# Kernel optimization log

Hardware: AMD Instinct MI355X
Metric: run time of the kernel (lower is better)

The kernel has to match this reference:

```python
import jax, jax.numpy as jnp
import numpy as np

B, C, H, W = 8, 256, 64, 64
EPS = 1e-5


def _mk_conv_bn(key, oc, ic):
    k = jax.random.split(key, 6)
    return dict(
        w=jax.random.normal(k[0], (oc, ic), jnp.float32) * 0.01,  # trunc-normal approx, stddev 0.01
        b=jnp.zeros((oc,), jnp.float32),
        s=jax.random.uniform(k[1], (oc,), jnp.float32, 0.5, 1.5),   # BN scale
        t=jax.random.normal(k[2], (oc,), jnp.float32) * 0.1,        # BN shift
        m=jax.random.normal(k[3], (oc,), jnp.float32) * 0.1,        # BN running mean
        v=jax.random.uniform(k[4], (oc,), jnp.float32, 0.5, 1.5),   # BN running var
    )


def setup_inputs() -> dict:
    key = jax.random.key(0)
    ks = jax.random.split(key, 6)
    d = {"x": jax.random.normal(ks[0], (B, C, H, W), jnp.float32)}
    for i, (oc, ic) in zip([1, 2, 3, 4], [(C // 8, C), (C // 8, C), (C // 2, C), (C, C // 2)]):
        p = _mk_conv_bn(ks[i], oc, ic)
        for name, val in p.items():
            d[f"{name}{i}"] = val
    d["gamma"] = jnp.asarray(0.5, jnp.float32)
    return d


def _cbn(x, w, b, s, t, m, v, relu=True):
    # conv1x1 + BatchNorm(eval) [+ ReLU]; dropout is identity at inference
    y = jnp.einsum('bchw,oc->bohw', x, w) + b[None, :, None, None]
    scale = (s / jnp.sqrt(v + EPS))[None, :, None, None]
    y = (y - m[None, :, None, None]) * scale + t[None, :, None, None]
    return jax.nn.relu(y) if relu else y


def _maxpool2(x):
    b, c, h, w = x.shape
    return x.reshape(b, c, h // 2, 2, w // 2, 2).max(axis=(3, 5))


def reference(x, w1, b1, s1, t1, m1, v1, w2, b2, s2, t2, m2, v2,
              w3, b3, s3, t3, m3, v3, w4, b4, s4, t4, m4, v4, gamma):
    b, c, h, w = x.shape
    f = _maxpool2(_cbn(x, w1, b1, s1, t1, m1, v1))   # (B, C/8, H/2, W/2)
    g = _cbn(x, w2, b2, s2, t2, m2, v2)              # (B, C/8, H, W)
    hh = _maxpool2(_cbn(x, w3, b3, s3, t3, m3, v3))  # (B, C/2, H/2, W/2)
    hw, hw4 = h * w, (h // 2) * (w // 2)
    f = f.reshape(b, c // 8, hw4).transpose(0, 2, 1)  # (B, HW/4, C/8)
    g = g.reshape(b, c // 8, hw)                      # (B, C/8, HW)
    s = jnp.einsum('bnk,bkm->bnm', f, g)              # (B, HW/4, HW)
    beta = jax.nn.softmax(s, axis=1)                  # softmax over dim=1, as in source
    hh = hh.reshape(b, c // 2, hw4)                   # (B, C/2, HW/4)
    o = jnp.einsum('bcn,bnm->bcm', hh, beta).reshape(b, c // 2, h, w)
    out = _cbn(o, w4, b4, s4, t4, m4, v4, relu=False)
    return gamma * out + x
```

## Files before the change

kernel.cpp:

```cpp
#include <hip/hip_runtime.h>
#include <hip/hip_bf16.h>

#define HW   4096
#define HW4  1024
#define EPS  1e-5f
#define SM_SHIFT 20.0f

typedef __attribute__((ext_vector_type(8)))  short    bf16x8;
typedef __attribute__((ext_vector_type(4)))  float    f32x4;

__device__ __forceinline__ short f2bs(float f) {
    union { float f; unsigned u; } v; v.f = f;
    unsigned r = v.u + 0x7FFFu + ((v.u >> 16) & 1u);
    return (short)(r >> 16);
}
__device__ __forceinline__ unsigned pk2(float a, float b) {
    unsigned r;
    asm("v_cvt_pk_bf16_f32 %0, %1, %2" : "=v"(r) : "v"(a), "v"(b));
    return r;
}
__device__ __forceinline__ int swz64(int r, int c)  { return (r << 6) + ((c ^ (r & 7))  << 3); }
__device__ __forceinline__ int swz128(int r, int c) { return (r << 7) + ((c ^ (r & 15)) << 3); }
__device__ __forceinline__ int p40(int r, int c)    { return r * 40 + c * 8; }

__device__ __forceinline__ void bar_lgk() {
    asm volatile("s_waitcnt lgkmcnt(0)" ::: "memory");
    __builtin_amdgcn_s_barrier();
    __builtin_amdgcn_sched_barrier(0);
}

__global__ __launch_bounds__(512) void conv123pool(
    const float* __restrict__ x,
    const float* __restrict__ w1, const float* __restrict__ b1, const float* __restrict__ s1,
    const float* __restrict__ t1, const float* __restrict__ m1, const float* __restrict__ v1,
    const float* __restrict__ w2, const float* __restrict__ b2, const float* __restrict__ s2,
    const float* __restrict__ t2, const float* __restrict__ m2, const float* __restrict__ v2,
    const float* __restrict__ w3, const float* __restrict__ b3, const float* __restrict__ s3,
    const float* __restrict__ t3, const float* __restrict__ m3, const float* __restrict__ v3,
    const float* __restrict__ w4,
    short* __restrict__ w4T,
    short* __restrict__ gbufT, short* __restrict__ fbufT, short* __restrict__ hhbuf)
{
    __shared__ __align__(16) short Wl[4 * 192 * 64];
    __shared__ __align__(16) short Xl[2 * 128 * 64];
    __shared__ float alB[192], beB[192];

    const int t = threadIdx.x;
    const int lane = t & 63, wv = t >> 6;
    const int quad = lane >> 4, l16 = lane & 15;
    const int ptile = blockIdx.x;
    const int bz    = blockIdx.y;
    const int pBase = ptile * 128;
    const int wcol  = (wv & 1) * 32;
    const int woch  = (wv >> 1) * 48;

    const int xp2 = (t & 63) * 2, xkg = t >> 6;
    const float* xBase = x + ((size_t)bz * 256 + xkg * 8) * HW + pBase + xp2;

    float2 fvA[8], fvB[8];
    #pragma unroll
    for (int j = 0; j < 8; ++j) fvA[j] = *(const float2*)(xBase + (size_t)j * HW);

    if (bz == 0) {
        int idx = (ptile * 512 + t) * 2;
        float2 a = *(const float2*)(w4 + idx);
        short2 o; o.x = f2bs(a.x); o.y = f2bs(a.y);
        *(short2*)&w4T[idx] = o;
    }

    if (t < 192) {
        int j = t;
        float pb, ps, ptv, pm, pv;
        if (j < 32)      { pb = b1[j]; ps = s1[j]; ptv = t1[j]; pm = m1[j]; pv = v1[j]; }
        else if (j < 64) { int c = j - 32; pb = b2[c]; ps = s2[c]; ptv = t2[c]; pm = m2[c]; pv = v2[c]; }
        else             { int c = j - 64; pb = b3[c]; ps = s3[c]; ptv = t3[c]; pm = m3[c]; pv = v3[c]; }
        float al = ps * rsqrtf(pv + EPS);
        alB[t] = al; beB[t] = (pb - pm) * al + ptv;
    }

    #pragma unroll
    for (int kc = 0; kc < 4; ++kc) {
        #pragma unroll
        for (int i = 0; i < 2; ++i) {
            int idx = t + i * 512;
            if (i == 0 || t < 256) {
                int oc = idx >> 2, kb = (idx & 3) * 16;
                const float* wp = (oc < 32) ? (w1 + oc * 256)
                                : (oc < 64) ? (w2 + (oc - 32) * 256)
                                            : (w3 + (oc - 64) * 256);
                wp += kc * 64 + kb;
                float4 a = *(const float4*)(wp);
                float4 b = *(const float4*)(wp + 4);
                float4 c = *(const float4*)(wp + 8);
                float4 d = *(const float4*)(wp + 12);
                bf16x8 lo, hi;
                lo[0]=f2bs(a.x); lo[1]=f2bs(a.y); lo[2]=f2bs(a.z); lo[3]=f2bs(a.w);
                lo[4]=f2bs(b.x); lo[5]=f2bs(b.y); lo[6]=f2bs(b.z); lo[7]=f2bs(b.w);
                hi[0]=f2bs(c.x); hi[1]=f2bs(c.y); hi[2]=f2bs(c.z); hi[3]=f2bs(c.w);
                hi[4]=f2bs(d.x); hi[5]=f2bs(d.y); hi[6]=f2bs(d.z); hi[7]=f2bs(d.w);
                *(bf16x8*)&Wl[kc * 12288 + swz64(oc, (kb >> 3))]     = lo;
                *(bf16x8*)&Wl[kc * 12288 + swz64(oc, (kb >> 3) + 1)] = hi;
            }
        }
    }

    const f32x4 fzero = {0.f, 0.f, 0.f, 0.f};
    f32x4 acc[3][4];
    #pragma unroll
    for (int i = 0; i < 3; ++i)
        #pragma unroll
        for (int j = 0; j < 4; ++j) acc[i][j] = fzero;

    const int ptOff0 = wcol, ptOff1 = wcol + 16, ptOff2 = wcol + 64, ptOff3 = wcol + 80;

#define K1_COMMIT(XB, CUR)                                                            \
    {   bf16x8 va, vb;                                                                \
        _Pragma("unroll")                                                             \
        for (int j2 = 0; j2 < 8; ++j2) { va[j2] = f2bs(CUR[j2].x); vb[j2] = f2bs(CUR[j2].y); } \
        *(bf16x8*)&Xl[(XB) * 8192 + swz64(xp2,     xkg)] = va;                        \
        *(bf16x8*)&Xl[(XB) * 8192 + swz64(xp2 + 1, xkg)] = vb;                        \
    }
#define K1_PREF(KC, NXT)                                                              \
    {   const float* xn = xBase + (size_t)((KC) * 64) * HW;                           \
        _Pragma("unroll")                                                             \
        for (int j2 = 0; j2 < 8; ++j2) NXT[j2] = *(const float2*)(xn + (size_t)j2 * HW); \
    }
#define K1_MFMA(XB, KC)                                                               \
    _Pragma("unroll")                                                                 \
    for (int kk = 0; kk < 2; ++kk) {                                                  \
        bf16x8 bfr[4];                                                                \
        bfr[0] = *(const bf16x8*)&Xl[(XB) * 8192 + swz64(ptOff0 + l16, kk * 4 + quad)]; \
        bfr[1] = *(const bf16x8*)&Xl[(XB) * 8192 + swz64(ptOff1 + l16, kk * 4 + quad)]; \
        bfr[2] = *(const bf16x8*)&Xl[(XB) * 8192 + swz64(ptOff2 + l16, kk * 4 + quad)]; \
        bfr[3] = *(const bf16x8*)&Xl[(XB) * 8192 + swz64(ptOff3 + l16, kk * 4 + quad)]; \
        _Pragma("unroll")                                                             \
        for (int tt = 0; tt < 3; ++tt) {                                              \
            bf16x8 afr = *(const bf16x8*)&Wl[(KC) * 12288 + swz64(woch + tt*16 + l16, kk*4 + quad)]; \
            _Pragma("unroll")                                                         \
            for (int pt = 0; pt < 4; ++pt)                                            \
                acc[tt][pt] = __builtin_amdgcn_mfma_f32_16x16x32_bf16(afr, bfr[pt], acc[tt][pt], 0, 0, 0); \
        }                                                                             \
    }

    K1_COMMIT(0, fvA)  K1_PREF(1, fvB)  bar_lgk();  K1_MFMA(0, 0)
    K1_COMMIT(1, fvB)  K1_PREF(2, fvA)  bar_lgk();  K1_MFMA(1, 1)
    K1_COMMIT(0, fvA)  K1_PREF(3, fvB)  bar_lgk();  K1_MFMA(0, 2)
    K1_COMMIT(1, fvB)                   bar_lgk();  K1_MFMA(1, 3)

#undef K1_COMMIT
#undef K1_PREF
#undef K1_MFMA

    #pragma unroll
    for (int tt = 0; tt < 3; ++tt) {
        #pragma unroll
        for (int r = 0; r < 4; ++r) {
            int j = woch + tt * 16 + quad * 4 + r;
            float al = alB[j], be = beB[j];
            float y[4];
            y[0] = fmaxf(acc[tt][0][r] * al + be, 0.f);
            y[1] = fmaxf(acc[tt][1][r] * al + be, 0.f);
            y[2] = fmaxf(acc[tt][2][r] * al + be, 0.f);
            y[3] = fmaxf(acc[tt][3][r] * al + be, 0.f);
            if (j >= 32 && j < 64) {
                size_t mb = (size_t)bz * 4096 + pBase;
                int kk = j - 32;
                gbufT[(mb + ptOff0 + l16) * 32 + kk] = f2bs(y[0]);
                gbufT[(mb + ptOff1 + l16) * 32 + kk] = f2bs(y[1]);
                gbufT[(mb + ptOff2 + l16) * 32 + kk] = f2bs(y[2]);
                gbufT[(mb + ptOff3 + l16) * 32 + kk] = f2bs(y[3]);
            } else {
                #pragma unroll
                for (int c = 0; c < 2; ++c) {
                    float v  = fmaxf(y[c], y[c + 2]);
                    float po = fmaxf(v, __shfl_xor(v, 1));
                    if ((l16 & 1) == 0) {
                        int col = wcol + c * 16 + l16;
                        int n = ptile * 32 + (col >> 1);
                        if (j < 32) fbufT[((size_t)bz * 1024 + n) * 32 + j] = f2bs(po);
                        else        hhbuf[((size_t)bz * 128 + (j - 64)) * HW4 + n] = f2bs(po);
                    }
                }
            }
        }
    }
}

__global__ __launch_bounds__(256, 2) void attn_conv4(
    const short* __restrict__ gbufT,
    const short* __restrict__ fbufT,
    const short* __restrict__ hhbuf,
    const float* __restrict__ x,
    const short* __restrict__ w4T, const float* __restrict__ b4, const float* __restrict__ s4,
    const float* __restrict__ t4, const float* __restrict__ m4, const float* __restrict__ v4,
    const float* __restrict__ gamma, float* __restrict__ out)
{
    __shared__ __align__(16) short smem[24576];
    __shared__ float alB4[256], beB4[256];
    __shared__ float Zl[128];
    short* o_l  = smem;
    short* Wl4  = smem + 8192;
    float* mrg  = (float*)(smem + 8192);
    short* sTp  = smem + (threadIdx.x >> 6) * 2560;

    const int t = threadIdx.x;
    const int lane = t & 63, wv = t >> 6;
    const int quad = lane >> 4, l16 = lane & 15;
    const int ci = wv >> 1, ni = wv & 1;
    const int nstrip = ni * 32, cbase = ci * 64;
    const int bz = blockIdx.y;
    const int m0 = blockIdx.x * 64;
    const f32x4 fzero = {0.f, 0.f, 0.f, 0.f};

    {
        float al = s4[t] * rsqrtf(v4[t] + EPS);
        alB4[t] = al; beB4[t] = (b4[t] - m4[t]) * al + t4[t];
    }

    const short* fT = fbufT + (size_t)bz * 1024 * 32;
    const short* hB = hhbuf + (size_t)bz * 128 * HW4;

    bf16x8 bg[4];
    #pragma unroll
    for (int mt = 0; mt < 4; ++mt)
        bg[mt] = *(const bf16x8*)&gbufT[((size_t)bz * 4096 + m0 + mt * 16 + l16) * 32 + quad * 8];

    bf16x8 frA[2], frB[2], hhA[4], hhB[4];
    frA[0] = *(const bf16x8*)&fT[(size_t)(nstrip + l16) * 32 + quad * 8];
    frA[1] = *(const bf16x8*)&fT[(size_t)(nstrip + 16 + l16) * 32 + quad * 8];
    #pragma unroll
    for (int ct = 0; ct < 4; ++ct)
        hhA[ct] = *(const bf16x8*)(hB + (size_t)(cbase + ct * 16 + l16) * HW4 + nstrip + quad * 8);

    float psum[4] = {0.f, 0.f, 0.f, 0.f};
    f32x4 oacc[4][4];
    #pragma unroll
    for (int a = 0; a < 4; ++a)
        #pragma unroll
        for (int b = 0; b < 4; ++b) oacc[a][b] = fzero;

    const int mr0 = l16 * 40, mr1 = (16 + l16) * 40, mr2 = (32 + l16) * 40, mr3 = (48 + l16) * 40;
    const int mrow[4] = {mr0, mr1, mr2, mr3};

    int n0n = 64;

#define ABODY(CURF, NXTF, CURH, NXTH)                                                 \
    {                                                                                 \
        f32x4 sacc0[4], sacc1[4];                                                     \
        _Pragma("unroll")                                                             \
        for (int mt = 0; mt < 4; ++mt)                                                \
            sacc0[mt] = __builtin_amdgcn_mfma_f32_16x16x32_bf16(CURF[0], bg[mt], fzero, 0, 0, 0); \
        _Pragma("unroll")                                                             \
        for (int mt = 0; mt < 4; ++mt)                                                \
            sacc1[mt] = __builtin_amdgcn_mfma_f32_16x16x32_bf16(CURF[1], bg[mt], fzero, 0, 0, 0); \
        NXTF[0] = *(const bf16x8*)&fT[(size_t)(n0n + nstrip + l16) * 32 + quad * 8];  \
        NXTF[1] = *(const bf16x8*)&fT[(size_t)(n0n + nstrip + 16 + l16) * 32 + quad * 8]; \
        _Pragma("unroll")                                                             \
        for (int mt = 0; mt < 4; ++mt) {                                              \
            float e0 = __expf(sacc0[mt][0] - SM_SHIFT);                               \
            float e1 = __expf(sacc0[mt][1] - SM_SHIFT);                               \
            float e2 = __expf(sacc0[mt][2] - SM_SHIFT);                               \
            float e3 = __expf(sacc0[mt][3] - SM_SHIFT);                               \
            float g0 = __expf(sacc1[mt][0] - SM_SHIFT);                               \
            float g1 = __expf(sacc1[mt][1] - SM_SHIFT);                               \
            float g2 = __expf(sacc1[mt][2] - SM_SHIFT);                               \
            float g3 = __expf(sacc1[mt][3] - SM_SHIFT);                               \
            psum[mt] += ((e0 + e1) + (e2 + e3)) + ((g0 + g1) + (g2 + g3));            \
            uint2 ev0; ev0.x = pk2(e0, e1); ev0.y = pk2(e2, e3);                      \
            uint2 ev1; ev1.x = pk2(g0, g1); ev1.y = pk2(g2, g3);                      \
            *(uint2*)&sTp[mrow[mt] + quad * 4]      = ev0;                            \
            *(uint2*)&sTp[mrow[mt] + 16 + quad * 4] = ev1;                            \
        }                                                                             \
        _Pragma("unroll")                                                             \
        for (int mt = 0; mt < 4; ++mt) {                                              \
            bf16x8 bfrag = *(const bf16x8*)&sTp[mrow[mt] + quad * 8];                 \
            _Pragma("unroll")                                                         \
            for (int ct = 0; ct < 4; ++ct)                                            \
                oacc[ct][mt] = __builtin_amdgcn_mfma_f32_16x16x32_bf16(CURH[ct], bfrag, oacc[ct][mt], 0, 0, 0); \
        }                                                                             \
        _Pragma("unroll")                                                             \
        for (int ct = 0; ct < 4; ++ct)                                                \
            NXTH[ct] = *(const bf16x8*)(hB + (size_t)(cbase + ct * 16 + l16) * HW4 + n0n + nstrip + quad * 8); \
        n0n = (n0n + 64) & 1023;                                                      \
    }

    for (int it2 = 0; it2 < 8; ++it2) {
        ABODY(frA, frB, hhA, hhB)
        ABODY(frB, frA, hhB, hhA)
    }
#undef ABODY

    #pragma unroll
    for (int mt = 0; mt < 4; ++mt) {
        psum[mt] += __shfl_xor(psum[mt], 16);
        psum[mt] += __shfl_xor(psum[mt], 32);
    }

    bar_lgk();

    if (ci == 0 && quad == 0) {
        #pragma unroll
        for (int mt = 0; mt < 4; ++mt) Zl[ni * 64 + mt * 16 + l16] = psum[mt];
    }
    if (ni == 1) {
        #pragma unroll
        for (int ct = 0; ct < 4; ++ct)
            #pragma unroll
            for (int mt = 0; mt < 4; ++mt)
                #pragma unroll
                for (int r = 0; r < 4; ++r)
                    mrg[(cbase + ct * 16 + quad * 4 + r) * 64 + mt * 16 + l16] = oacc[ct][mt][r];
    }
    bar_lgk();

    if (ni == 0) {
        #pragma unroll
        for (int mt = 0; mt < 4; ++mt) {
            float iv = 1.0f / (Zl[mt * 16 + l16] + Zl[64 + mt * 16 + l16]);
            #pragma unroll
            for (int ct = 0; ct < 4; ++ct) {
                short4 ov;
                #pragma unroll
                for (int r = 0; r < 4; ++r) {
                    float v = oacc[ct][mt][r]
                            + mrg[(cbase + ct * 16 + quad * 4 + r) * 64 + mt * 16 + l16];
                    ((short*)&ov)[r] = f2bs(v * iv);
                }
                *(short4*)&o_l[swz128(mt * 16 + l16, ci * 8 + ct * 2 + (quad >> 1)) + (quad & 1) * 4] = ov;
            }
        }
    }

    f32x4 acc4[4][4];
    #pragma unroll
    for (int i = 0; i < 4; ++i)
        #pragma unroll
        for (int j = 0; j < 4; ++j) acc4[i][j] = fzero;

    const int wrow = t >> 2, wcid = t & 3;
    bf16x8 Wr[4];
    #pragma unroll
    for (int g = 0; g < 4; ++g)
        Wr[g] = *(const bf16x8*)(w4T + (g * 64 + wrow) * 128 + wcid * 8);

    #pragma unroll
    for (int k0i = 0; k0i < 4; ++k0i) {
        const int k0 = k0i * 32;
        bar_lgk();
        #pragma unroll
        for (int g = 0; g < 4; ++g)
            *(bf16x8*)&Wl4[p40(g * 64 + wrow, wcid)] = Wr[g];
        if (k0i < 3) {
            #pragma unroll
            for (int g = 0; g < 4; ++g)
                Wr[g] = *(const bf16x8*)(w4T + (g * 64 + wrow) * 128 + k0 + 32 + wcid * 8);
        }
        bar_lgk();
        bf16x8 bfr[4];
        #pragma unroll
        for (int mt = 0; mt < 4; ++mt)
            bfr[mt] = *(const bf16x8*)&o_l[swz128(mt * 16 + l16, (k0 >> 3) + quad)];
        #pragma unroll
        for (int ot = 0; ot < 4; ++ot) {
            bf16x8 afr = *(const bf16x8*)&Wl4[p40(wv * 64 + ot * 16 + l16, quad)];
            #pragma unroll
            for (int mt = 0; mt < 4; ++mt)
                acc4[ot][mt] = __builtin_amdgcn_mfma_f32_16x16x32_bf16(afr, bfr[mt], acc4[ot][mt], 0, 0, 0);
        }
    }

    float gm = gamma[0];
    #pragma unroll
    for (int ot = 0; ot < 4; ++ot) {
        #pragma unroll
        for (int r = 0; r < 4; ++r) {
            int oc = wv * 64 + ot * 16 + quad * 4 + r;
            float al = alB4[oc], be = beB4[oc];
            #pragma unroll
            for (int mt = 0; mt < 4; ++mt) {
                int p = m0 + mt * 16 + l16;
                float y  = acc4[ot][mt][r] * al + be;
                float xo = x[((size_t)bz * 256 + oc) * HW + p];
                out[((size_t)bz * 256 + oc) * HW + p] = gm * y + xo;
            }
        }
    }
}

extern "C" void kernel_launch(void* const* d_in, const int* in_sizes, int n_in,
                              void* d_out, int out_size, void* d_ws, size_t ws_size,
                              hipStream_t stream)
{
    const float* x  = (const float*)d_in[0];
    const float* w1 = (const float*)d_in[1];
    const float* b1 = (const float*)d_in[2];
    const float* s1 = (const float*)d_in[3];
    const float* t1 = (const float*)d_in[4];
    const float* m1 = (const float*)d_in[5];
    const float* v1 = (const float*)d_in[6];
    const float* w2 = (const float*)d_in[7];
    const float* b2 = (const float*)d_in[8];
    const float* s2 = (const float*)d_in[9];
    const float* t2 = (const float*)d_in[10];
    const float* m2 = (const float*)d_in[11];
    const float* v2 = (const float*)d_in[12];
    const float* w3 = (const float*)d_in[13];
    const float* b3 = (const float*)d_in[14];
    const float* s3 = (const float*)d_in[15];
    const float* t3 = (const float*)d_in[16];
    const float* m3 = (const float*)d_in[17];
    const float* v3 = (const float*)d_in[18];
    const float* w4 = (const float*)d_in[19];
    const float* b4 = (const float*)d_in[20];
    const float* s4 = (const float*)d_in[21];
    const float* t4 = (const float*)d_in[22];
    const float* m4 = (const float*)d_in[23];
    const float* v4 = (const float*)d_in[24];
    const float* gm = (const float*)d_in[25];
    float* out = (float*)d_out;

    short* gbufT = (short*)d_ws;
    short* fbufT = gbufT + (size_t)8 * 4096 * 32;
    short* hhbuf = fbufT + (size_t)8 * 1024 * 32;
    short* w4T   = hhbuf + (size_t)8 * 128 * 1024;

    conv123pool<<<dim3(32, 8), 512, 0, stream>>>(
        x, w1, b1, s1, t1, m1, v1, w2, b2, s2, t2, m2, v2, w3, b3, s3, t3, m3, v3,
        w4, w4T, gbufT, fbufT, hhbuf);
    attn_conv4<<<dim3(64, 8), 256, 0, stream>>>(
        gbufT, fbufT, hhbuf, x, w4T, b4, s4, t4, m4, v4, gm, out);
}
```

Baseline: 164.8 us.

## Compute softmax denominators via MFMA with ones, use packed bf16 converts

Replaces the per-lane scalar exp-sum accumulation and cross-lane shuffle reduction with an extra MFMA per tile that multiplies a ones fragment by the bf16 probability fragment. The column sums then come out of the matrix core and stay consistent with the rounded bf16 values used in the PV product. Software bf16 rounding in the projection kernel is swapped for the packed v_cvt_pk_bf16_f32 instruction. The attention kernel's occupancy hint is dropped and the custom barriers become __syncthreads. The extra MFMA adds matrix-core work, and relaxing launch bounds may change register allocation and occupancy.

```diff
diff --git a/kernel.cpp b/kernel.cpp
--- a/kernel.cpp
+++ b/kernel.cpp
@@ -8,6 +8,7 @@
 
 typedef __attribute__((ext_vector_type(8)))  short    bf16x8;
 typedef __attribute__((ext_vector_type(4)))  float    f32x4;
+typedef __attribute__((ext_vector_type(4)))  unsigned u32x4;
 
 __device__ __forceinline__ short f2bs(float f) {
     union { float f; unsigned u; } v; v.f = f;
@@ -64,8 +65,8 @@
     if (bz == 0) {
         int idx = (ptile * 512 + t) * 2;
         float2 a = *(const float2*)(w4 + idx);
-        short2 o; o.x = f2bs(a.x); o.y = f2bs(a.y);
-        *(short2*)&w4T[idx] = o;
+        unsigned o = pk2(a.x, a.y);
+        *(unsigned*)&w4T[idx] = o;
     }
 
     if (t < 192) {
@@ -93,13 +94,10 @@
                 float4 b = *(const float4*)(wp + 4);
                 float4 c = *(const float4*)(wp + 8);
                 float4 d = *(const float4*)(wp + 12);
-                bf16x8 lo, hi;
-                lo[0]=f2bs(a.x); lo[1]=f2bs(a.y); lo[2]=f2bs(a.z); lo[3]=f2bs(a.w);
-                lo[4]=f2bs(b.x); lo[5]=f2bs(b.y); lo[6]=f2bs(b.z); lo[7]=f2bs(b.w);
-                hi[0]=f2bs(c.x); hi[1]=f2bs(c.y); hi[2]=f2bs(c.z); hi[3]=f2bs(c.w);
-                hi[4]=f2bs(d.x); hi[5]=f2bs(d.y); hi[6]=f2bs(d.z); hi[7]=f2bs(d.w);
-                *(bf16x8*)&Wl[kc * 12288 + swz64(oc, (kb >> 3))]     = lo;
-                *(bf16x8*)&Wl[kc * 12288 + swz64(oc, (kb >> 3) + 1)] = hi;
+                *(u32x4*)&Wl[kc * 12288 + swz64(oc, (kb >> 3))] =
+                    (u32x4){pk2(a.x,a.y), pk2(a.z,a.w), pk2(b.x,b.y), pk2(b.z,b.w)};
+                *(u32x4*)&Wl[kc * 12288 + swz64(oc, (kb >> 3) + 1)] =
+                    (u32x4){pk2(c.x,c.y), pk2(c.z,c.w), pk2(d.x,d.y), pk2(d.z,d.w)};
             }
         }
     }
@@ -114,11 +112,14 @@
     const int ptOff0 = wcol, ptOff1 = wcol + 16, ptOff2 = wcol + 64, ptOff3 = wcol + 80;
 
 #define K1_COMMIT(XB, CUR)                                                            \
-    {   bf16x8 va, vb;                                                                \
-        _Pragma("unroll")                                                             \
-        for (int j2 = 0; j2 < 8; ++j2) { va[j2] = f2bs(CUR[j2].x); vb[j2] = f2bs(CUR[j2].y); } \
-        *(bf16x8*)&Xl[(XB) * 8192 + swz64(xp2,     xkg)] = va;                        \
-        *(bf16x8*)&Xl[(XB) * 8192 + swz64(xp2 + 1, xkg)] = vb;                        \
+    {   u32x4 va, vb;                                                                 \
+        _Pragma("unroll")                                                             \
+        for (int w2i = 0; w2i < 4; ++w2i) {                                           \
+            va[w2i] = pk2(CUR[2*w2i].x, CUR[2*w2i+1].x);                              \
+            vb[w2i] = pk2(CUR[2*w2i].y, CUR[2*w2i+1].y);                              \
+        }                                                                             \
+        *(u32x4*)&Xl[(XB) * 8192 + swz64(xp2,     xkg)] = va;                         \
+        *(u32x4*)&Xl[(XB) * 8192 + swz64(xp2 + 1, xkg)] = vb;                         \
     }
 #define K1_PREF(KC, NXT)                                                              \
     {   const float* xn = xBase + (size_t)((KC) * 64) * HW;                           \
@@ -186,7 +187,7 @@
     }
 }
 
-__global__ __launch_bounds__(256, 2) void attn_conv4(
+__global__ __launch_bounds__(256) void attn_conv4(
     const short* __restrict__ gbufT,
     const short* __restrict__ fbufT,
     const short* __restrict__ hhbuf,
@@ -225,6 +226,10 @@
     for (int mt = 0; mt < 4; ++mt)
         bg[mt] = *(const bf16x8*)&gbufT[((size_t)bz * 4096 + m0 + mt * 16 + l16) * 32 + quad * 8];
 
+    bf16x8 ONESF;
+    #pragma unroll
+    for (int j = 0; j < 8; ++j) ONESF[j] = (short)0x3F80;
+
     bf16x8 frA[2], frB[2], hhA[4], hhB[4];
     frA[0] = *(const bf16x8*)&fT[(size_t)(nstrip + l16) * 32 + quad * 8];
     frA[1] = *(const bf16x8*)&fT[(size_t)(nstrip + 16 + l16) * 32 + quad * 8];
@@ -232,12 +237,14 @@
     for (int ct = 0; ct < 4; ++ct)
         hhA[ct] = *(const bf16x8*)(hB + (size_t)(cbase + ct * 16 + l16) * HW4 + nstrip + quad * 8);
 
-    float psum[4] = {0.f, 0.f, 0.f, 0.f};
+    f32x4 zacc[4];
     f32x4 oacc[4][4];
     #pragma unroll
-    for (int a = 0; a < 4; ++a)
+    for (int a = 0; a < 4; ++a) {
+        zacc[a] = fzero;
         #pragma unroll
         for (int b = 0; b < 4; ++b) oacc[a][b] = fzero;
+    }
 
     const int mr0 = l16 * 40, mr1 = (16 + l16) * 40, mr2 = (32 + l16) * 40, mr3 = (48 + l16) * 40;
     const int mrow[4] = {mr0, mr1, mr2, mr3};
@@ -265,7 +272,6 @@
             float g1 = __expf(sacc1[mt][1] - SM_SHIFT);                               \
             float g2 = __expf(sacc1[mt][2] - SM_SHIFT);                               \
             float g3 = __expf(sacc1[mt][3] - SM_SHIFT);                               \
-            psum[mt] += ((e0 + e1) + (e2 + e3)) + ((g0 + g1) + (g2 + g3));            \
             uint2 ev0; ev0.x = pk2(e0, e1); ev0.y = pk2(e2, e3);                      \
             uint2 ev1; ev1.x = pk2(g0, g1); ev1.y = pk2(g2, g3);                      \
             *(uint2*)&sTp[mrow[mt] + quad * 4]      = ev0;                            \
@@ -277,6 +283,7 @@
             _Pragma("unroll")                                                         \
             for (int ct = 0; ct < 4; ++ct)                                            \
                 oacc[ct][mt] = __builtin_amdgcn_mfma_f32_16x16x32_bf16(CURH[ct], bfrag, oacc[ct][mt], 0, 0, 0); \
+            zacc[mt] = __builtin_amdgcn_mfma_f32_16x16x32_bf16(ONESF, bfrag, zacc[mt], 0, 0, 0); \
         }                                                                             \
         _Pragma("unroll")                                                             \
         for (int ct = 0; ct < 4; ++ct)                                                \
@@ -290,17 +297,11 @@
     }
 #undef ABODY
 
-    #pragma unroll
-    for (int mt = 0; mt < 4; ++mt) {
-        psum[mt] += __shfl_xor(psum[mt], 16);
-        psum[mt] += __shfl_xor(psum[mt], 32);
-    }
-
-    bar_lgk();
+    __syncthreads();
 
     if (ci == 0 && quad == 0) {
         #pragma unroll
-        for (int mt = 0; mt < 4; ++mt) Zl[ni * 64 + mt * 16 + l16] = psum[mt];
+        for (int mt = 0; mt < 4; ++mt) Zl[ni * 64 + mt * 16 + l16] = zacc[mt][0];
     }
     if (ni == 1) {
         #pragma unroll
@@ -311,7 +312,7 @@
                 for (int r = 0; r < 4; ++r)
                     mrg[(cbase + ct * 16 + quad * 4 + r) * 64 + mt * 16 + l16] = oacc[ct][mt][r];
     }
-    bar_lgk();
+    __syncthreads();
 
     if (ni == 0) {
         #pragma unroll
@@ -346,7 +347,7 @@
     #pragma unroll
     for (int k0i = 0; k0i < 4; ++k0i) {
         const int k0 = k0i * 32;
-        bar_lgk();
+        __syncthreads();
         #pragma unroll
         for (int g = 0; g < 4; ++g)
             *(bf16x8*)&Wl4[p40(g * 64 + wrow, wcid)] = Wr[g];
@@ -355,7 +356,7 @@
             for (int g = 0; g < 4; ++g)
                 Wr[g] = *(const bf16x8*)(w4T + (g * 64 + wrow) * 128 + k0 + 32 + wcid * 8);
         }
-        bar_lgk();
+        __syncthreads();
         bf16x8 bfr[4];
         #pragma unroll
         for (int mt = 0; mt < 4; ++mt)
```

New measurement: 168.7 us. 2.4% more time.
